# Performance work log

Measured on AMD Instinct MI355X. Metric: run time of the kernel, lower is better.

The kernel has to match this reference:

```python
import jax, jax.numpy as jnp
import numpy as np

N, K, M, C, OUT, S = 80000, 8, 1000, 128, 64, 2
EPS = 1e-5


def _bn(x, g, b, m, v):
    # eval-mode BatchNorm1d applied over the last (channel) axis
    return (x - m) * (g / jnp.sqrt(v + EPS)) + b


def setup_inputs() -> dict:
    key = jax.random.key(0)
    ks = jax.random.split(key, 40)
    it = iter(range(40))
    rn = lambda sh, s=1.0: jax.random.normal(ks[next(it)], sh, dtype=jnp.float32) * s
    ru = lambda sh: jax.random.uniform(ks[next(it)], sh, dtype=jnp.float32, minval=0.5, maxval=1.5)
    w = 0.05
    inp = {}
    inp["sp_fea"] = rn((M, C))
    inp["sp_xyz"] = rn((M, 3))
    inp["o_p_fea"] = rn((N, C))
    inp["p_xyz"] = rn((N, 3))
    # linear_q / linear_k / linear_v  (in_planes -> mid_planes)
    inp["Wq"] = rn((C, C), w); inp["bq"] = jnp.zeros((C,), jnp.float32)
    inp["Wk"] = rn((C, C), w); inp["bk"] = jnp.zeros((C,), jnp.float32)
    inp["Wv"] = rn((C, C), w); inp["bv"] = jnp.zeros((C,), jnp.float32)
    # linear_p: Linear(3,3) -> BN(3) -> ReLU -> Linear(3, mid)
    inp["Wp1"] = rn((3, 3), 0.5); inp["bp1"] = jnp.zeros((3,), jnp.float32)
    inp["gp"] = 1.0 + rn((3,), 0.1); inp["betap"] = rn((3,), 0.1)
    inp["mp"] = rn((3,), 0.1); inp["vp"] = ru((3,))
    inp["Wp2"] = rn((3, C), 0.3); inp["bp2"] = jnp.zeros((C,), jnp.float32)
    # linear_w: BN(mid) -> ReLU -> Linear(mid,out) -> BN(out) -> ReLU -> Linear(out,out)
    inp["g1"] = 1.0 + rn((C,), 0.1); inp["beta1"] = rn((C,), 0.1)
    inp["m1"] = rn((C,), 0.1); inp["v1"] = ru((C,))
    inp["W1"] = rn((C, OUT), w); inp["b1"] = jnp.zeros((OUT,), jnp.float32)
    inp["g2"] = 1.0 + rn((OUT,), 0.1); inp["beta2"] = rn((OUT,), 0.1)
    inp["m2"] = rn((OUT,), 0.1); inp["v2"] = ru((OUT,))
    inp["W2"] = rn((OUT, OUT), w); inp["b2"] = jnp.zeros((OUT,), jnp.float32)
    # index / offset inputs (ints)
    inp["c2p_idx_abs"] = jax.random.randint(ks[next(it)], (N, K), 0, M)
    inp["c2p_idx"] = jax.random.randint(ks[next(it)], (N, K), 0, M)
    inp["cluster_idx"] = jax.random.randint(ks[next(it)], (N,), 0, M)
    inp["offset"] = jnp.array([N], dtype=jnp.int32)
    inp["sp_offset"] = jnp.array([M], dtype=jnp.int32)
    return inp


def reference(sp_fea, sp_xyz, o_p_fea, p_xyz,
              Wq, bq, Wk, bk, Wv, bv,
              Wp1, bp1, gp, betap, mp, vp, Wp2, bp2,
              g1, beta1, m1, v1, W1, b1,
              g2, beta2, m2, v2, W2, b2,
              c2p_idx_abs, c2p_idx, cluster_idx, offset, sp_offset):
    q = o_p_fea @ Wq + bq                               # [N, C]
    k_sp = (sp_fea @ Wk + bk)[c2p_idx_abs]              # gather -> [N, K, C]
    v_sp = (sp_fea @ Wv + bv)[c2p_idx_abs]              # [N, K, C]
    p_e = sp_xyz[c2p_idx_abs]                           # [N, K, 3]
    # positional encoding MLP
    p_e = jax.nn.relu(_bn(p_e @ Wp1 + bp1, gp, betap, mp, vp)) @ Wp2 + bp2  # [N, K, C]
    # vector attention scores
    w = k_sp - q[:, None, :] + p_e                      # [N, K, C]
    w = jax.nn.relu(_bn(w, g1, beta1, m1, v1)) @ W1 + b1
    w = jax.nn.relu(_bn(w, g2, beta2, m2, v2)) @ W2 + b2  # [N, K, OUT]
    w = jax.nn.softmax(w, axis=1)                        # softmax over the K neighbors
    # shared-plane weighted sum
    bi = ((v_sp + p_e).reshape(N, K, S, C // S) * w[:, :, None, :]).reshape(N, K, C)
    bi = bi.sum(axis=2)                                  # [N, K]
    return jax.nn.softmax(bi, axis=1)                    # association matrix [N, K]
```

## Files before the change

kernel.cpp:

```cpp
#include <hip/hip_runtime.h>
#include <stdint.h>

#define EPS 1e-5f

#define NPTS 80000
#define CDIM 128
#define ODIM 64
#define KNBR 8
#define MSUP 1000

#define KP2H_OFF 0
#define UT_OFF   (256*1024)
#define WQF_OFF  (512*1024)
#define W1F_OFF  (544*1024)
#define W2F_OFF  (560*1024)
#define C1_OFF   (568*1024)
#define WSTAGE_BYTES (16*1024 + 8*1024 + 256)

typedef float f32x4 __attribute__((ext_vector_type(4)));
typedef short bf16x8 __attribute__((ext_vector_type(8)));

union FragU { bf16x8 v; unsigned u[4]; uint4 q; };

#if __has_builtin(__builtin_amdgcn_cvt_pk_bf16_f32)
typedef __bf16 bf16x2_t __attribute__((ext_vector_type(2)));
#define HAVE_PK_BF16 1
#endif

__device__ inline unsigned pk_bf16(float lo, float hi) {
#ifdef HAVE_PK_BF16
  return __builtin_bit_cast(unsigned, __builtin_amdgcn_cvt_pk_bf16_f32(lo, hi));
#else
  unsigned a = __builtin_bit_cast(unsigned, lo);
  unsigned b = __builtin_bit_cast(unsigned, hi);
  a += 0x7FFFu + ((a >> 16) & 1u);
  b += 0x7FFFu + ((b >> 16) & 1u);
  return (a >> 16) | (b & 0xFFFF0000u);
#endif
}

__device__ inline void unpk(unsigned p, float& lo, float& hi) {
  lo = __builtin_bit_cast(float, p << 16);
  hi = __builtin_bit_cast(float, p & 0xFFFF0000u);
}

__global__ __launch_bounds__(256)
void k_prep(const float* __restrict__ sp_fea, const float* __restrict__ sp_xyz,
            const float* __restrict__ Wk, const float* __restrict__ bk,
            const float* __restrict__ Wv, const float* __restrict__ bv,
            const float* __restrict__ Wp1, const float* __restrict__ bp1,
            const float* __restrict__ gp, const float* __restrict__ betap,
            const float* __restrict__ mp, const float* __restrict__ vp,
            const float* __restrict__ Wp2, const float* __restrict__ bp2,
            const float* __restrict__ g1, const float* __restrict__ beta1,
            const float* __restrict__ m1, const float* __restrict__ v1,
            const float* __restrict__ bq,
            const float* __restrict__ Wq, const float* __restrict__ W1,
            const float* __restrict__ W2,
            const float* __restrict__ g2, const float* __restrict__ v2,
            const float* __restrict__ b1, const float* __restrict__ m2,
            const float* __restrict__ beta2, char* __restrict__ ws)
{
  if (blockIdx.x < 1000) {
    unsigned short* kp2h = (unsigned short*)(ws + KP2H_OFF);
    float* uT = (float*)(ws + UT_OFF);
    const int m = blockIdx.x;
    const int t = threadIdx.x;
    const int c = t & 127, half = t >> 7;
    __shared__ float fea[128];
    __shared__ float pk[128], pv[128];
    if (t < 128) fea[t] = sp_fea[m * 128 + t];
    __syncthreads();
    float kv = 0.f, vv = 0.f;
    const float* wkc = Wk + half * 64 * 128 + c;
    const float* wvc = Wv + half * 64 * 128 + c;
    const float* feah = fea + half * 64;
    #pragma unroll 8
    for (int d = 0; d < 64; ++d) {
      const float f = feah[d];
      kv = fmaf(f, wkc[d * 128], kv);
      vv = fmaf(f, wvc[d * 128], vv);
    }
    if (half) { pk[c] = kv; pv[c] = vv; }
    __syncthreads();
    if (!half) {
      kv += pk[c] + bk[c];
      vv += pv[c] + bv[c];
      const float x0 = sp_xyz[m*3+0], x1 = sp_xyz[m*3+1], x2 = sp_xyz[m*3+2];
      float pe = bp2[c];
      #pragma unroll
      for (int ii = 0; ii < 3; ++ii) {
        float s = bp1[ii] + x0*Wp1[0*3+ii] + x1*Wp1[1*3+ii] + x2*Wp1[2*3+ii];
        s = (s - mp[ii]) * (gp[ii] * rsqrtf(vp[ii] + EPS)) + betap[ii];
        s = fmaxf(s, 0.0f);
        pe += s * Wp2[ii*128 + c];
      }
      const float s1c = g1[c] * rsqrtf(v1[c] + EPS);
      const float kpv = (kv + pe - m1[c] - bq[c]) * s1c + beta1[c];
      kp2h[m*128 + c] = (unsigned short)(pk_bf16(kpv, kpv) & 0xFFFFu);
      pv[c] = vv + pe;
    }
    __syncthreads();
    if (t < 64) uT[m*64 + t] = pv[t] + pv[t + 64];
  } else {
    const int tid = (blockIdx.x - 1000) * 256 + threadIdx.x;
    if (tid < 2048) {
      const int e = tid, f = e >> 6, l = e & 63;
      const int kt = f >> 3, mt = f & 7;
      const int c = mt*16 + (l & 15);
      const int d0 = kt*32 + (l >> 4)*8;
      const float sc = g1[c] * rsqrtf(v1[c] + EPS);
      uint4 u;
      u.x = pk_bf16(Wq[(d0+0)*128 + c]*sc, Wq[(d0+1)*128 + c]*sc);
      u.y = pk_bf16(Wq[(d0+2)*128 + c]*sc, Wq[(d0+3)*128 + c]*sc);
      u.z = pk_bf16(Wq[(d0+4)*128 + c]*sc, Wq[(d0+5)*128 + c]*sc);
      u.w = pk_bf16(Wq[(d0+6)*128 + c]*sc, Wq[(d0+7)*128 + c]*sc);
      *(uint4*)(ws + WQF_OFF + e*16) = u;
    } else if (tid < 3072) {
      const int e = tid - 2048, f = e >> 6, l = e & 63;
      const int kt = f >> 2, jt = f & 3;
      const int j = jt*16 + (l & 15);
      const int c0 = kt*32 + (l >> 4)*8;
      const float sc = g2[j] * rsqrtf(v2[j] + EPS);
      uint4 u;
      u.x = pk_bf16(W1[(c0+0)*64 + j]*sc, W1[(c0+1)*64 + j]*sc);
      u.y = pk_bf16(W1[(c0+2)*64 + j]*sc, W1[(c0+3)*64 + j]*sc);
      u.z = pk_bf16(W1[(c0+4)*64 + j]*sc, W1[(c0+5)*64 + j]*sc);
      u.w = pk_bf16(W1[(c0+6)*64 + j]*sc, W1[(c0+7)*64 + j]*sc);
      *(uint4*)(ws + W1F_OFF + e*16) = u;
    } else if (tid < 3584) {
      const int e = tid - 3072, f = e >> 6, l = e & 63;
      const int kt2 = f >> 2, nt = f & 3;
      const int jp = nt*16 + (l & 15);
      const int j0 = kt2*32 + (l >> 4)*8;
      uint4 u;
      u.x = pk_bf16(W2[(j0+0)*64 + jp], W2[(j0+1)*64 + jp]);
      u.y = pk_bf16(W2[(j0+2)*64 + jp], W2[(j0+3)*64 + jp]);
      u.z = pk_bf16(W2[(j0+4)*64 + jp], W2[(j0+5)*64 + jp]);
      u.w = pk_bf16(W2[(j0+6)*64 + jp], W2[(j0+7)*64 + jp]);
      *(uint4*)(ws + W2F_OFF + e*16) = u;
    } else if (tid < 3648) {
      const int j = tid - 3584;
      const float sc = g2[j] * rsqrtf(v2[j] + EPS);
      ((float*)(ws + C1_OFF))[j] = (b1[j] - m2[j]) * sc + beta2[j];
    }
  }
}

#define QS_PITCH 272
#define QS_SIZE  (16*272)
#define H2_PITCH 144
#define H2_SIZE  (16*144)
#define W1L_OFF  0
#define W2L_OFF  (16*1024)
#define C1L_OFF  (24*1024)
#define QS_BASE  24832
#define H2_BASE  (24832 + 2*QS_SIZE)
#define LDS_TOTAL (H2_BASE + 2*H2_SIZE)

__global__ __launch_bounds__(128, 2)
void k_main(const float* __restrict__ o_p_fea, const int* __restrict__ idx,
            const float* __restrict__ b2, const char* __restrict__ ws,
            float* __restrict__ out)
{
  const unsigned short* kp2h = (const unsigned short*)(ws + KP2H_OFF);
  const float*  uT  = (const float*)(ws + UT_OFF);
  const bf16x8* wqf = (const bf16x8*)(ws + WQF_OFF);

  __shared__ __align__(16) char lds[LDS_TOTAL];
  const int t = threadIdx.x;
  const int wave = t >> 6;
  const int l = t & 63;
  const int quad = l >> 4, row = l & 15;
  char* qs_w = lds + QS_BASE + wave * QS_SIZE;
  char* h2_w = lds + H2_BASE + wave * H2_SIZE;

  const int sg = blockIdx.x * 2 + wave;
  const int n0 = sg * 16;
  const int idx_base = n0 * 8;

  {
    const uint4* src = (const uint4*)(ws + W1F_OFF);
    uint4* dst = (uint4*)lds;
    #pragma unroll
    for (int i = 0; i < 13; ++i) {
      const int e = t + i * 128;
      if (e < WSTAGE_BYTES / 16) dst[e] = src[e];
    }
  }

  int mr8[8];
  #pragma unroll
  for (int g = 0; g < 8; ++g) mr8[g] = idx[idx_base + g*16 + row];

  {
    f32x4 qa[8];
    #pragma unroll
    for (int mt = 0; mt < 8; ++mt) qa[mt] = (f32x4){0.f, 0.f, 0.f, 0.f};
    const float* feab = o_p_fea + (size_t)(n0 + row) * 128;
    #pragma unroll
    for (int kt = 0; kt < 4; ++kt) {
      f32x4 fa = *(const f32x4*)(feab + kt*32 + quad*8);
      f32x4 fb = *(const f32x4*)(feab + kt*32 + quad*8 + 4);
      FragU bu;
      bu.u[0] = pk_bf16(fa[0], fa[1]);
      bu.u[1] = pk_bf16(fa[2], fa[3]);
      bu.u[2] = pk_bf16(fb[0], fb[1]);
      bu.u[3] = pk_bf16(fb[2], fb[3]);
      #pragma unroll
      for (int mt = 0; mt < 8; ++mt)
        qa[mt] = __builtin_amdgcn_mfma_f32_16x16x32_bf16(wqf[(kt*8+mt)*64 + l], bu.v, qa[mt], 0, 0, 0);
    }
    #pragma unroll
    for (int mt = 0; mt < 8; ++mt) {
      uint2 pp;
      pp.x = pk_bf16(qa[mt][0], qa[mt][1]);
      pp.y = pk_bf16(qa[mt][2], qa[mt][3]);
      *(uint2*)(qs_w + row*QS_PITCH + (mt*16 + quad*4)*2) = pp;
    }
  }

  __syncthreads();

  f32x4 c1r[4];
  #pragma unroll
  for (int jt = 0; jt < 4; ++jt)
    c1r[jt] = *(const f32x4*)(lds + C1L_OFF + (jt*16 + quad*4)*4);
  float b2r[4];
  #pragma unroll
  for (int nt = 0; nt < 4; ++nt) b2r[nt] = b2[row + nt*16];

  uint4 kfc[4], kfn[4];
  {
    const uint4* kr = (const uint4*)(kp2h + (size_t)mr8[0] * 128);
    #pragma unroll
    for (int kt = 0; kt < 4; ++kt) kfc[kt] = kr[kt*4 + quad];
  }

  #pragma unroll 1
  for (int g = 0; g < 8; ++g) {
    const int m_r = mr8[g];
    if (g < 7) {
      const uint4* kr = (const uint4*)(kp2h + (size_t)mr8[g+1] * 128);
      #pragma unroll
      for (int kt = 0; kt < 4; ++kt) kfn[kt] = kr[kt*4 + quad];
    }
    int msrc[4];
    #pragma unroll
    for (int rg = 0; rg < 4; ++rg) msrc[rg] = __shfl(m_r, quad*4 + rg);
    float u4[4][4];
    #pragma unroll
    for (int rg = 0; rg < 4; ++rg) {
      const float* ur = uT + (size_t)msrc[rg] * 64 + row;
      #pragma unroll
      for (int nt = 0; nt < 4; ++nt) u4[rg][nt] = ur[nt*16];
    }

    const int nloc = row >> 3;
    const char* qrow = qs_w + (g*2 + nloc) * QS_PITCH;

    f32x4 a1[4];
    #pragma unroll
    for (int jt = 0; jt < 4; ++jt) a1[jt] = (f32x4){0.f, 0.f, 0.f, 0.f};
    #pragma unroll
    for (int kt = 0; kt < 4; ++kt) {
      const uint4 kp = kfc[kt];
      const uint4 qp = *(const uint4*)(qrow + kt*64 + quad*16);
      FragU xf;
      {
        float klo, khi, qlo, qhi;
        unpk(kp.x, klo, khi); unpk(qp.x, qlo, qhi);
        xf.u[0] = pk_bf16(fmaxf(klo - qlo, 0.f), fmaxf(khi - qhi, 0.f));
        unpk(kp.y, klo, khi); unpk(qp.y, qlo, qhi);
        xf.u[1] = pk_bf16(fmaxf(klo - qlo, 0.f), fmaxf(khi - qhi, 0.f));
        unpk(kp.z, klo, khi); unpk(qp.z, qlo, qhi);
        xf.u[2] = pk_bf16(fmaxf(klo - qlo, 0.f), fmaxf(khi - qhi, 0.f));
        unpk(kp.w, klo, khi); unpk(qp.w, qlo, qhi);
        xf.u[3] = pk_bf16(fmaxf(klo - qlo, 0.f), fmaxf(khi - qhi, 0.f));
      }
      #pragma unroll
      for (int jt = 0; jt < 4; ++jt) {
        const bf16x8 wf = *(const bf16x8*)(lds + W1L_OFF + (kt*4+jt)*1024 + l*16);
        a1[jt] = __builtin_amdgcn_mfma_f32_16x16x32_bf16(wf, xf.v, a1[jt], 0, 0, 0);
      }
    }
    #pragma unroll
    for (int kt = 0; kt < 4; ++kt) kfc[kt] = kfn[kt];

    #pragma unroll
    for (int jt = 0; jt < 4; ++jt) {
      f32x4 v = a1[jt] + c1r[jt];
      uint2 pp;
      pp.x = pk_bf16(fmaxf(v[0], 0.f), fmaxf(v[1], 0.f));
      pp.y = pk_bf16(fmaxf(v[2], 0.f), fmaxf(v[3], 0.f));
      *(uint2*)(h2_w + row*H2_PITCH + (jt*16 + quad*4)*2) = pp;
    }

    f32x4 a2[4];
    #pragma unroll
    for (int nt = 0; nt < 4; ++nt) a2[nt] = (f32x4){0.f, 0.f, 0.f, 0.f};
    #pragma unroll
    for (int kt2 = 0; kt2 < 2; ++kt2) {
      const bf16x8 af = *(const bf16x8*)(h2_w + row*H2_PITCH + kt2*64 + quad*16);
      #pragma unroll
      for (int nt = 0; nt < 4; ++nt) {
        const bf16x8 wf = *(const bf16x8*)(lds + W2L_OFF + (kt2*4+nt)*1024 + l*16);
        a2[nt] = __builtin_amdgcn_mfma_f32_16x16x32_bf16(af, wf, a2[nt], 0, 0, 0);
      }
    }
    float e[4][4], rs[4];
    #pragma unroll
    for (int nt = 0; nt < 4; ++nt) {
      #pragma unroll
      for (int rg = 0; rg < 4; ++rg) e[nt][rg] = __expf(a2[nt][rg] + b2r[nt]);
      float s = e[nt][0] + e[nt][1] + e[nt][2] + e[nt][3];
      s += __shfl_xor(s, 16);
      rs[nt] = __builtin_amdgcn_rcpf(s);
    }
    float bi[4] = {0.f, 0.f, 0.f, 0.f};
    #pragma unroll
    for (int rg = 0; rg < 4; ++rg) {
      #pragma unroll
      for (int nt = 0; nt < 4; ++nt)
        bi[rg] = fmaf(e[nt][rg] * rs[nt], u4[rg][nt], bi[rg]);
    }
    #pragma unroll
    for (int rg = 0; rg < 4; ++rg) {
      float b = bi[rg];
      b += __shfl_xor(b, 1);
      b += __shfl_xor(b, 2);
      b += __shfl_xor(b, 4);
      b += __shfl_xor(b, 8);
      bi[rg] = b;
    }
    const float eb0 = __expf(bi[0]), eb1 = __expf(bi[1]);
    const float eb2 = __expf(bi[2]), eb3 = __expf(bi[3]);
    float sb = eb0 + eb1 + eb2 + eb3;
    sb += __shfl_xor(sb, 16);
    const float rsb = __builtin_amdgcn_rcpf(sb);
    if (row < 4) {
      const float vsel = row == 0 ? eb0 : row == 1 ? eb1 : row == 2 ? eb2 : eb3;
      out[n0*8 + g*16 + quad*4 + row] = vsel * rsb;
    }
  }
}

extern "C" void kernel_launch(void* const* d_in, const int* in_sizes, int n_in,
                              void* d_out, int out_size, void* d_ws, size_t ws_size,
                              hipStream_t stream)
{
  const float* sp_fea  = (const float*)d_in[0];
  const float* sp_xyz  = (const float*)d_in[1];
  const float* o_p_fea = (const float*)d_in[2];
  const float* Wq    = (const float*)d_in[4];
  const float* bq    = (const float*)d_in[5];
  const float* Wk    = (const float*)d_in[6];
  const float* bk    = (const float*)d_in[7];
  const float* Wv    = (const float*)d_in[8];
  const float* bv    = (const float*)d_in[9];
  const float* Wp1   = (const float*)d_in[10];
  const float* bp1   = (const float*)d_in[11];
  const float* gp    = (const float*)d_in[12];
  const float* betap = (const float*)d_in[13];
  const float* mp    = (const float*)d_in[14];
  const float* vp    = (const float*)d_in[15];
  const float* Wp2   = (const float*)d_in[16];
  const float* bp2   = (const float*)d_in[17];
  const float* g1    = (const float*)d_in[18];
  const float* beta1 = (const float*)d_in[19];
  const float* m1    = (const float*)d_in[20];
  const float* v1    = (const float*)d_in[21];
  const float* W1    = (const float*)d_in[22];
  const float* b1    = (const float*)d_in[23];
  const float* g2    = (const float*)d_in[24];
  const float* beta2 = (const float*)d_in[25];
  const float* m2    = (const float*)d_in[26];
  const float* v2    = (const float*)d_in[27];
  const float* W2    = (const float*)d_in[28];
  const float* b2    = (const float*)d_in[29];
  const int* c2p_idx_abs = (const int*)d_in[30];

  char* ws = (char*)d_ws;
  float* out = (float*)d_out;

  hipLaunchKernelGGL(k_prep, dim3(1015), dim3(256), 0, stream,
                     sp_fea, sp_xyz, Wk, bk, Wv, bv, Wp1, bp1, gp, betap, mp, vp,
                     Wp2, bp2, g1, beta1, m1, v1, bq,
                     Wq, W1, W2, g2, v2, b1, m2, beta2, ws);
  hipLaunchKernelGGL(k_main, dim3(2500), dim3(128), 0, stream,
                     o_p_fea, c2p_idx_abs, b2, ws, out);
}
```

Before: 224.8 us.

## Split Q projection into separate kernel and prefetch q rows from global

Moves the per-point Q projection MFMA out of the main kernel into its own kernel, which writes bf16 q rows to workspace. The main kernel now uses 256-thread blocks with four waves. It prefetches the next group's q fragments and neighbor indices from global memory alongside the k fragments, rather than reading q from LDS and broadcasting indices with shuffles. This shrinks main-kernel LDS and registers to allow more waves in flight. The cost is an extra launch plus a 20 MB write and read-back of q through global memory.

```diff
diff --git a/kernel.cpp b/kernel.cpp
--- a/kernel.cpp
+++ b/kernel.cpp
@@ -15,6 +15,7 @@
 #define W1F_OFF  (544*1024)
 #define W2F_OFF  (560*1024)
 #define C1_OFF   (568*1024)
+#define QSG_OFF  (576*1024)
 #define WSTAGE_BYTES (16*1024 + 8*1024 + 256)
 
 typedef float f32x4 __attribute__((ext_vector_type(4)));
@@ -147,44 +148,75 @@
   }
 }
 
-#define QS_PITCH 272
-#define QS_SIZE  (16*272)
+__global__ __launch_bounds__(256, 4)
+void k_q(const float* __restrict__ o_p_fea, char* __restrict__ ws)
+{
+  const bf16x8* wqf = (const bf16x8*)(ws + WQF_OFF);
+  char* qs_g = ws + QSG_OFF;
+  const int t = threadIdx.x;
+  const int wave = t >> 6, l = t & 63;
+  const int quad = l >> 4, row = l & 15;
+  const int n0 = (blockIdx.x * 4 + wave) * 16;
+
+  f32x4 qa[8];
+  #pragma unroll
+  for (int mt = 0; mt < 8; ++mt) qa[mt] = (f32x4){0.f, 0.f, 0.f, 0.f};
+  const float* feab = o_p_fea + (size_t)(n0 + row) * 128;
+  #pragma unroll
+  for (int kt = 0; kt < 4; ++kt) {
+    f32x4 fa = *(const f32x4*)(feab + kt*32 + quad*8);
+    f32x4 fb = *(const f32x4*)(feab + kt*32 + quad*8 + 4);
+    FragU bu;
+    bu.u[0] = pk_bf16(fa[0], fa[1]);
+    bu.u[1] = pk_bf16(fa[2], fa[3]);
+    bu.u[2] = pk_bf16(fb[0], fb[1]);
+    bu.u[3] = pk_bf16(fb[2], fb[3]);
+    #pragma unroll
+    for (int mt = 0; mt < 8; ++mt)
+      qa[mt] = __builtin_amdgcn_mfma_f32_16x16x32_bf16(wqf[(kt*8+mt)*64 + l], bu.v, qa[mt], 0, 0, 0);
+  }
+  #pragma unroll
+  for (int mt = 0; mt < 8; ++mt) {
+    uint2 pp;
+    pp.x = pk_bf16(qa[mt][0], qa[mt][1]);
+    pp.y = pk_bf16(qa[mt][2], qa[mt][3]);
+    *(uint2*)(qs_g + (size_t)(n0 + row) * 256 + mt*32 + quad*8) = pp;
+  }
+}
+
 #define H2_PITCH 144
 #define H2_SIZE  (16*144)
 #define W1L_OFF  0
 #define W2L_OFF  (16*1024)
 #define C1L_OFF  (24*1024)
-#define QS_BASE  24832
-#define H2_BASE  (24832 + 2*QS_SIZE)
-#define LDS_TOTAL (H2_BASE + 2*H2_SIZE)
-
-__global__ __launch_bounds__(128, 2)
-void k_main(const float* __restrict__ o_p_fea, const int* __restrict__ idx,
-            const float* __restrict__ b2, const char* __restrict__ ws,
-            float* __restrict__ out)
+#define H2_BASE  24832
+#define LDS_TOTAL (H2_BASE + 4*H2_SIZE)
+
+__global__ __launch_bounds__(256, 3)
+void k_main(const int* __restrict__ idx, const float* __restrict__ b2,
+            const char* __restrict__ ws, float* __restrict__ out)
 {
   const unsigned short* kp2h = (const unsigned short*)(ws + KP2H_OFF);
-  const float*  uT  = (const float*)(ws + UT_OFF);
-  const bf16x8* wqf = (const bf16x8*)(ws + WQF_OFF);
+  const float* uT = (const float*)(ws + UT_OFF);
+  const char* qs_g = ws + QSG_OFF;
 
   __shared__ __align__(16) char lds[LDS_TOTAL];
   const int t = threadIdx.x;
-  const int wave = t >> 6;
-  const int l = t & 63;
+  const int wave = t >> 6, l = t & 63;
   const int quad = l >> 4, row = l & 15;
-  char* qs_w = lds + QS_BASE + wave * QS_SIZE;
   char* h2_w = lds + H2_BASE + wave * H2_SIZE;
 
-  const int sg = blockIdx.x * 2 + wave;
+  const int sg = blockIdx.x * 4 + wave;
   const int n0 = sg * 16;
   const int idx_base = n0 * 8;
+  const int nloc = row >> 3;
 
   {
     const uint4* src = (const uint4*)(ws + W1F_OFF);
     uint4* dst = (uint4*)lds;
     #pragma unroll
-    for (int i = 0; i < 13; ++i) {
-      const int e = t + i * 128;
+    for (int i = 0; i < 7; ++i) {
+      const int e = t + i * 256;
       if (e < WSTAGE_BYTES / 16) dst[e] = src[e];
     }
   }
@@ -192,33 +224,6 @@
   int mr8[8];
   #pragma unroll
   for (int g = 0; g < 8; ++g) mr8[g] = idx[idx_base + g*16 + row];
-
-  {
-    f32x4 qa[8];
-    #pragma unroll
-    for (int mt = 0; mt < 8; ++mt) qa[mt] = (f32x4){0.f, 0.f, 0.f, 0.f};
-    const float* feab = o_p_fea + (size_t)(n0 + row) * 128;
-    #pragma unroll
-    for (int kt = 0; kt < 4; ++kt) {
-      f32x4 fa = *(const f32x4*)(feab + kt*32 + quad*8);
-      f32x4 fb = *(const f32x4*)(feab + kt*32 + quad*8 + 4);
-      FragU bu;
-      bu.u[0] = pk_bf16(fa[0], fa[1]);
-      bu.u[1] = pk_bf16(fa[2], fa[3]);
-      bu.u[2] = pk_bf16(fb[0], fb[1]);
-      bu.u[3] = pk_bf16(fb[2], fb[3]);
-      #pragma unroll
-      for (int mt = 0; mt < 8; ++mt)
-        qa[mt] = __builtin_amdgcn_mfma_f32_16x16x32_bf16(wqf[(kt*8+mt)*64 + l], bu.v, qa[mt], 0, 0, 0);
-    }
-    #pragma unroll
-    for (int mt = 0; mt < 8; ++mt) {
-      uint2 pp;
-      pp.x = pk_bf16(qa[mt][0], qa[mt][1]);
-      pp.y = pk_bf16(qa[mt][2], qa[mt][3]);
-      *(uint2*)(qs_w + row*QS_PITCH + (mt*16 + quad*4)*2) = pp;
-    }
-  }
 
   __syncthreads();
 
@@ -230,34 +235,36 @@
   #pragma unroll
   for (int nt = 0; nt < 4; ++nt) b2r[nt] = b2[row + nt*16];
 
-  uint4 kfc[4], kfn[4];
+  int msc[4];
+  #pragma unroll
+  for (int rg = 0; rg < 4; ++rg) msc[rg] = idx[idx_base + quad*4 + rg];
+  uint4 kfc[4], qpc[4];
   {
     const uint4* kr = (const uint4*)(kp2h + (size_t)mr8[0] * 128);
-    #pragma unroll
-    for (int kt = 0; kt < 4; ++kt) kfc[kt] = kr[kt*4 + quad];
+    const uint4* qr = (const uint4*)(qs_g + (size_t)(n0 + nloc) * 256);
+    #pragma unroll
+    for (int kt = 0; kt < 4; ++kt) { kfc[kt] = kr[kt*4 + quad]; qpc[kt] = qr[kt*4 + quad]; }
   }
 
   #pragma unroll 1
   for (int g = 0; g < 8; ++g) {
-    const int m_r = mr8[g];
+    int msn[4];
+    uint4 kfn[4], qpn[4];
     if (g < 7) {
+      #pragma unroll
+      for (int rg = 0; rg < 4; ++rg) msn[rg] = idx[idx_base + (g+1)*16 + quad*4 + rg];
       const uint4* kr = (const uint4*)(kp2h + (size_t)mr8[g+1] * 128);
-      #pragma unroll
-      for (int kt = 0; kt < 4; ++kt) kfn[kt] = kr[kt*4 + quad];
-    }
-    int msrc[4];
-    #pragma unroll
-    for (int rg = 0; rg < 4; ++rg) msrc[rg] = __shfl(m_r, quad*4 + rg);
+      const uint4* qr = (const uint4*)(qs_g + (size_t)(n0 + (g+1)*2 + nloc) * 256);
+      #pragma unroll
+      for (int kt = 0; kt < 4; ++kt) { kfn[kt] = kr[kt*4 + quad]; qpn[kt] = qr[kt*4 + quad]; }
+    }
     float u4[4][4];
     #pragma unroll
     for (int rg = 0; rg < 4; ++rg) {
-      const float* ur = uT + (size_t)msrc[rg] * 64 + row;
+      const float* ur = uT + (size_t)msc[rg] * 64 + row;
       #pragma unroll
       for (int nt = 0; nt < 4; ++nt) u4[rg][nt] = ur[nt*16];
     }
-
-    const int nloc = row >> 3;
-    const char* qrow = qs_w + (g*2 + nloc) * QS_PITCH;
 
     f32x4 a1[4];
     #pragma unroll
@@ -265,7 +272,7 @@
     #pragma unroll
     for (int kt = 0; kt < 4; ++kt) {
       const uint4 kp = kfc[kt];
-      const uint4 qp = *(const uint4*)(qrow + kt*64 + quad*16);
+      const uint4 qp = qpc[kt];
       FragU xf;
       {
         float klo, khi, qlo, qhi;
@@ -284,8 +291,6 @@
         a1[jt] = __builtin_amdgcn_mfma_f32_16x16x32_bf16(wf, xf.v, a1[jt], 0, 0, 0);
       }
     }
-    #pragma unroll
-    for (int kt = 0; kt < 4; ++kt) kfc[kt] = kfn[kt];
 
     #pragma unroll
     for (int jt = 0; jt < 4; ++jt) {
@@ -341,6 +346,12 @@
     if (row < 4) {
       const float vsel = row == 0 ? eb0 : row == 1 ? eb1 : row == 2 ? eb2 : eb3;
       out[n0*8 + g*16 + quad*4 + row] = vsel * rsb;
+    }
+    if (g < 7) {
+      #pragma unroll
+      for (int rg = 0; rg < 4; ++rg) msc[rg] = msn[rg];
+      #pragma unroll
+      for (int kt = 0; kt < 4; ++kt) { kfc[kt] = kfn[kt]; qpc[kt] = qpn[kt]; }
     }
   }
 }
@@ -387,6 +398,8 @@
                      sp_fea, sp_xyz, Wk, bk, Wv, bv, Wp1, bp1, gp, betap, mp, vp,
                      Wp2, bp2, g1, beta1, m1, v1, bq,
                      Wq, W1, W2, g2, v2, b1, m2, beta2, ws);
-  hipLaunchKernelGGL(k_main, dim3(2500), dim3(128), 0, stream,
-                     o_p_fea, c2p_idx_abs, b2, ws, out);
-}
+  hipLaunchKernelGGL(k_q, dim3(1250), dim3(256), 0, stream,
+                     o_p_fea, ws);
+  hipLaunchKernelGGL(k_main, dim3(1250), dim3(256), 0, stream,
+                     c2p_idx_abs, b2, ws, out);
+}
```

New measurement: 221.5 us. About the same (-1.4%).
